# Optimization experiments

Hardware: AMD Instinct MI355X
Metric: run time of the kernel (lower is better)

The kernel has to match this reference:

```python
import jax, jax.numpy as jnp
import numpy as np

N_NODES = 50000
N_EDGES = 800000
IN_CH = 64
HID = 64
N_LAYERS = 3
K = 16           # num_clusters
OUT_CH = 64
MAX_DEG = 512
M_SUB = 256
F_CAT = HID * N_LAYERS  # 192, jk concat width
EPS = 1e-5


def graph_norm(x, w, b, ms):
    # PyG GraphNorm over all nodes (single graph): shift by ms*mean, scale by std
    mu = jnp.mean(x, axis=0)
    sh = x - ms * mu
    var = jnp.mean(sh * sh, axis=0)
    return w * sh / jnp.sqrt(var + EPS) + b


def _lin(k, fi, fo):
    k1, k2 = jax.random.split(k)
    lim = 1.0 / np.sqrt(fi)
    W = jax.random.uniform(k1, (fi, fo), minval=-lim, maxval=lim, dtype=jnp.float32)
    b = jax.random.uniform(k2, (fo,), minval=-lim, maxval=lim, dtype=jnp.float32)
    return W, b


def setup_inputs() -> dict:
    key = jax.random.key(0)
    ks = jax.random.split(key, 20)
    x = jax.random.randint(ks[0], (N_NODES,), 0, MAX_DEG + 1)
    edge_index = jax.random.randint(ks[1], (2, N_EDGES), 0, N_NODES)
    edge_weight = jax.random.uniform(ks[2], (N_EDGES,), dtype=jnp.float32)
    pos = jax.random.randint(ks[3], (M_SUB,), 0, N_NODES)
    subgraph_assignment = jax.random.uniform(ks[4], (M_SUB, N_NODES), dtype=jnp.float32)
    emb_table = jax.random.normal(ks[5], (MAX_DEG + 1, IN_CH), dtype=jnp.float32)
    conv_Ws, conv_bs = [], []
    for l in range(N_LAYERS):
        W, b = _lin(jax.random.fold_in(ks[6], l), IN_CH if l == 0 else HID, HID)
        conv_Ws.append(W); conv_bs.append(b)
    conv_W = jnp.stack(conv_Ws); conv_b = jnp.stack(conv_bs)
    gn_w = jnp.ones((N_LAYERS - 1, HID)) + 0.05 * jax.random.normal(ks[7], (N_LAYERS - 1, HID))
    gn_b = 0.05 * jax.random.normal(ks[8], (N_LAYERS - 1, HID))
    gn_ms = jnp.ones((N_LAYERS - 1, HID)) + 0.05 * jax.random.normal(ks[9], (N_LAYERS - 1, HID))
    gnl_w = jnp.ones((F_CAT,)) + 0.05 * jax.random.normal(ks[10], (F_CAT,))
    gnl_b = 0.05 * jax.random.normal(ks[11], (F_CAT,))
    gnl_ms = jnp.ones((F_CAT,)) + 0.05 * jax.random.normal(ks[12], (F_CAT,))
    emb_gn_w = jnp.ones((IN_CH,)) + 0.05 * jax.random.normal(ks[13], (IN_CH,))
    emb_gn_b = 0.05 * jax.random.normal(ks[14], (IN_CH,))
    emb_gn_ms = jnp.ones((IN_CH,)) + 0.05 * jax.random.normal(ks[15], (IN_CH,))
    s_W, s_b = _lin(ks[16], F_CAT, K)
    pin = (F_CAT + 1) * K
    p_W1, p_b1 = _lin(jax.random.fold_in(ks[17], 0), pin, 2 * HID)
    p_W2, p_b2 = _lin(jax.random.fold_in(ks[17], 1), 2 * HID, 2 * HID)
    p_W3, p_b3 = _lin(jax.random.fold_in(ks[17], 2), 2 * HID, 2 * HID)
    p_W4, p_b4 = _lin(jax.random.fold_in(ks[17], 3), 2 * HID, OUT_CH)
    return dict(x=x, edge_index=edge_index, edge_weight=edge_weight, pos=pos,
                subgraph_assignment=subgraph_assignment, emb_table=emb_table,
                emb_gn_w=emb_gn_w, emb_gn_b=emb_gn_b, emb_gn_ms=emb_gn_ms,
                conv_W=conv_W, conv_b=conv_b, gn_w=gn_w, gn_b=gn_b, gn_ms=gn_ms,
                gnl_w=gnl_w, gnl_b=gnl_b, gnl_ms=gnl_ms, s_W=s_W, s_b=s_b,
                p_W1=p_W1, p_b1=p_b1, p_W2=p_W2, p_b2=p_b2,
                p_W3=p_W3, p_b3=p_b3, p_W4=p_W4, p_b4=p_b4)


def reference(x, edge_index, edge_weight, pos, subgraph_assignment,
              emb_table, emb_gn_w, emb_gn_b, emb_gn_ms,
              conv_W, conv_b, gn_w, gn_b, gn_ms,
              gnl_w, gnl_b, gnl_ms, s_W, s_b,
              p_W1, p_b1, p_W2, p_b2, p_W3, p_b3, p_W4, p_b4):
    n = x.shape[0]
    row, col = edge_index[0], edge_index[1]
    # buildAdj, aggr='mean': row-normalized weights with zero-degree bump
    deg_raw = jax.ops.segment_sum(edge_weight, row, num_segments=n)
    deg = jnp.where(deg_raw < 0.5, deg_raw + 1.0, deg_raw)
    norm_w = edge_weight / deg[row]
    # input embedding + GraphNorm
    h = graph_norm(emb_table[x], emb_gn_w, emb_gn_b, emb_gn_ms)
    xs = []
    for l in range(N_LAYERS):
        # GLASSConv: relu(Linear(x)) then normalized-adj SpMM (dropout off: eval)
        h = jax.nn.relu(h @ conv_W[l] + conv_b[l])
        h = jax.ops.segment_sum(norm_w[:, None] * h[col], row, num_segments=n)
        xs.append(h)
        if l < N_LAYERS - 1:
            h = jax.nn.relu(graph_norm(h, gn_w[l], gn_b[l], gn_ms[l]))
    hcat = graph_norm(jnp.concatenate(xs, axis=-1), gnl_w, gnl_b, gnl_ms)  # [N, F_CAT]
    s = hcat @ s_W + s_b                       # [N, K] cluster logits
    s_sm = jax.nn.softmax(s, axis=-1)
    # dense_mincut_pool (losses via edge list == dense adj formulation)
    out = s_sm.T @ hcat                        # [K, F_CAT]
    mincut_num = jnp.sum(edge_weight * jnp.sum(s_sm[row] * s_sm[col], axis=-1))
    mincut_den = jnp.sum(deg_raw * jnp.sum(s_sm * s_sm, axis=-1))
    mc_loss = -(mincut_num / mincut_den)
    ss = s_sm.T @ s_sm                         # [K, K]
    o_loss = jnp.linalg.norm(ss / jnp.linalg.norm(ss) - jnp.eye(K) / jnp.sqrt(K))
    # subgraph -> cluster soft assignment: L1-normalize softmax(s)^T rows
    t = s_sm.T
    t = t / jnp.maximum(jnp.sum(jnp.abs(t), axis=1, keepdims=True), 1e-12)
    sub2clu = t @ subgraph_assignment.T        # [K, M]
    def pool_one(r):
        # concat cluster score column, sort clusters by score descending, flatten
        xcat = jnp.concatenate([out, r[:, None]], axis=-1)  # [K, F_CAT+1]
        return xcat[jnp.argsort(-r)].reshape(-1)
    emb = jax.vmap(pool_one)(sub2clu.T)        # [M, K*(F_CAT+1)]
    h1 = jax.nn.relu(emb @ p_W1 + p_b1)
    h2 = jax.nn.relu(h1 @ p_W2 + p_b2)
    h3 = jax.nn.relu(h2 @ p_W3 + p_b3)
    pred = h3 @ p_W4 + p_b4                    # [M, OUT_CH]
    return pred, mc_loss, o_loss
```

## Files before the change

kernel.cpp:

```cpp
#include <hip/hip_runtime.h>
#include <hip/hip_bf16.h>

using bf16 = __hip_bfloat16;

constexpr int NN  = 50000;
constexpr int NE  = 800000;
constexpr int MS  = 256;
constexpr int FC  = 192;
constexpr int KC  = 16;
constexpr int PIN = 3088;
constexpr double EPSC = 1e-5;

static __device__ __forceinline__ double ldv(const bf16* p, size_t i){ return (double)__bfloat162float(p[i]); }
static __device__ __forceinline__ double ldv(const float* p, size_t i){ return (double)p[i]; }

__global__ void k_probe(const unsigned int* __restrict__ w, int* __restrict__ flag){
  __shared__ int red[256];
  int t=threadIdx.x, mx=0;
  for (int k=t;k<512;k+=256){
    unsigned int v=w[k];
    int e=(int)((v>>7)&0xFF);
    mx = e>mx? e:mx;
  }
  red[t]=mx; __syncthreads();
  for (int s=128;s;s>>=1){ if(t<s) red[t]=max(red[t],red[t+s]); __syncthreads(); }
  if (t==0) *flag = (red[0] <= 140) ? 1 : 0;
}

struct Seg { const void* src; double* dst; float* dstf; int cnt; int off; };
struct CvtArgs { Seg s[24]; int n; int total; };
__global__ void k_convert(CvtArgs a, const int* __restrict__ flag){
  int f=*flag;
  int stride=gridDim.x*blockDim.x;
  for (int idx=blockIdx.x*blockDim.x+threadIdx.x; idx<a.total; idx+=stride){
    int lo=0;
    while (idx >= a.s[lo].off + a.s[lo].cnt) lo++;
    int j = idx - a.s[lo].off;
    double v = f ? (double)__bfloat162float(((const bf16*)a.s[lo].src)[j])
                 : (double)((const float*)a.s[lo].src)[j];
    a.s[lo].dst[j]=v;
    if (a.s[lo].dstf) a.s[lo].dstf[j]=(float)v;
  }
}

__global__ void k_reduce_d(const double* __restrict__ part, int nb, int C, double* __restrict__ out){
  __shared__ double sh[256];
  int c=blockIdx.x;
  int t=threadIdx.x;
  double s=0.0;
  for (int b=t;b<nb;b+=256) s+=part[(size_t)b*C+c];
  sh[t]=s; __syncthreads();
  for (int w=128;w;w>>=1){ if(t<w) sh[t]+=sh[t+w]; __syncthreads(); }
  if (t==0) out[c]=sh[0];
}

__global__ void k_cnt(const int* __restrict__ ei, int* __restrict__ cnt){
  int stride=gridDim.x*blockDim.x;
  for (int e=blockIdx.x*blockDim.x+threadIdx.x; e<NE; e+=stride)
    atomicAdd(&cnt[ei[e]],1);
}

__global__ void k_scan_a(const int* __restrict__ cnt, int* __restrict__ rowptr,
                         int* __restrict__ bsum){
  __shared__ int s[256];
  int t=threadIdx.x; int i=blockIdx.x*256+t;
  int v=(i<NN)?cnt[i]:0;
  s[t]=v; __syncthreads();
  for (int off=1;off<256;off<<=1){
    int x=(t>=off)?s[t-off]:0; __syncthreads();
    s[t]+=x; __syncthreads();
  }
  if (i<NN) rowptr[i]=s[t]-v;
  if (t==255) bsum[blockIdx.x]=s[255];
}
__global__ void k_scan_b(int* __restrict__ bsum, int nb){
  __shared__ int s[256];
  int t=threadIdx.x;
  int v=(t<nb)?bsum[t]:0;
  s[t]=v; __syncthreads();
  for (int off=1;off<256;off<<=1){
    int x=(t>=off)?s[t-off]:0; __syncthreads();
    s[t]+=x; __syncthreads();
  }
  if (t<nb) bsum[t]=s[t]-v;
}
__global__ void k_scan_c(int* __restrict__ rowptr, const int* __restrict__ bsum,
                         int* __restrict__ cursor){
  int i=blockIdx.x*256+threadIdx.x;
  if (i<NN){ int v=rowptr[i]+bsum[blockIdx.x]; rowptr[i]=v; cursor[i]=v; }
  if (i==0) rowptr[NN]=NE;
}

template<typename T>
__device__ __forceinline__ void scat_body(const int* __restrict__ ei, const T* __restrict__ ew,
                                          int* __restrict__ cursor, int* __restrict__ ccol,
                                          double* __restrict__ cw, int* __restrict__ ceid){
  int stride=gridDim.x*blockDim.x;
  for (int e=blockIdx.x*blockDim.x+threadIdx.x; e<NE; e+=stride){
    int r=ei[e], c=ei[NE+e];
    int p=atomicAdd(&cursor[r],1);
    ccol[p]=c; cw[p]=ldv(ew,e); ceid[p]=e;
  }
}
__global__ void k_scatter(const int* ei, const void* ew, const int* flag,
                          int* cursor, int* ccol, double* cw, int* ceid){
  if (*flag) scat_body(ei,(const bf16*)ew,cursor,ccol,cw,ceid);
  else       scat_body(ei,(const float*)ew,cursor,ccol,cw,ceid);
}

__global__ void k_rowfix(const int* __restrict__ rowptr, int* __restrict__ ccol,
                         double* __restrict__ cw, int* __restrict__ ceid,
                         double* __restrict__ deg){
  int r=blockIdx.x*blockDim.x+threadIdx.x;
  if (r>=NN) return;
  int r0=rowptr[r], r1=rowptr[r+1];
  for (int k=r0;k<r1;k++){
    int best=ceid[k], bi=k;
    for (int e=k+1;e<r1;e++){ int id=ceid[e]; if (id<best){best=id;bi=e;} }
    if (bi!=k){
      int te=ceid[k]; ceid[k]=ceid[bi]; ceid[bi]=te;
      int tc=ccol[k]; ccol[k]=ccol[bi]; ccol[bi]=tc;
      double tw=cw[k]; cw[k]=cw[bi]; cw[bi]=tw;
    }
  }
  double d=0.0;
  for (int k=r0;k<r1;k++) d+=cw[k];
  deg[r]=d;
  double dn=(d<0.5)?d+1.0:d;
  for (int k=r0;k<r1;k++) cw[k]=cw[k]/dn;
}

__global__ void k_emb(const int* __restrict__ x, const double* __restrict__ tab,
                      double* __restrict__ h, double* __restrict__ part){
  __shared__ double r1[256], r2[256];
  int t=threadIdx.x; int stride=gridDim.x*blockDim.x;
  double s1=0.0,s2=0.0;
  for (int idx=blockIdx.x*blockDim.x+t; idx<NN*64; idx+=stride){
    int i=idx>>6, c=idx&63;
    double v=tab[x[i]*64+c];
    h[idx]=v; s1+=v; s2+=v*v;
  }
  r1[t]=s1; r2[t]=s2; __syncthreads();
  if (t<64){
    double a=r1[t]+r1[t+64]+r1[t+128]+r1[t+192];
    double b=r2[t]+r2[t+64]+r2[t+128]+r2[t+192];
    part[(size_t)blockIdx.x*128+t]=a;
    part[(size_t)blockIdx.x*128+64+t]=b;
  }
}

__global__ void k_gnfin(const double* __restrict__ S,
                        const double* __restrict__ w, const double* __restrict__ b,
                        const double* __restrict__ ms, int C,
                        double* __restrict__ A, double* __restrict__ B){
  int c=threadIdx.x; if (c>=C) return;
  const double inv_n=1.0/(double)NN;
  double m1=S[c]*inv_n, ex2=S[c+C]*inv_n;
  double cc=ms[c]*m1;
  double var=ex2-2.0*cc*m1+cc*cc;
  double a=w[c]/sqrt(var+EPSC);
  A[c]=a; B[c]=b[c]-a*cc;
}

__global__ void k_gnfin_jk(const double* __restrict__ S3,
                           const double* __restrict__ w, const double* __restrict__ b,
                           const double* __restrict__ ms,
                           double* __restrict__ A, double* __restrict__ B){
  int c=threadIdx.x; if (c>=192) return;
  int l=c>>6, cc=c&63;
  const double inv_n=1.0/(double)NN;
  double m1=S3[l*128+cc]*inv_n, ex2=S3[l*128+64+cc]*inv_n;
  double m=ms[c]*m1;
  double var=ex2-2.0*m*m1+m*m;
  double a=w[c]/sqrt(var+EPSC);
  A[c]=a; B[c]=b[c]-a*m;
}

__global__ void __launch_bounds__(256) k_lin64gn(
        const double* __restrict__ X, int ldx, int cx, int inRelu,
        const double* __restrict__ A, const double* __restrict__ Bb,
        const double* __restrict__ W, const double* __restrict__ bias,
        double* __restrict__ out){
  __shared__ double Wl[4096];
  __shared__ double Al[64], Bl[64];
  int t=threadIdx.x;
  for (int i=t;i<4096;i+=256) Wl[i]=W[i];
  if (t<64){ Al[t]=A[t]; Bl[t]=Bb[t]; }
  __syncthreads();
  int lane=t&63;
  int wid=blockIdx.x*4+(t>>6);
  int nw=gridDim.x*4;
  double bj=bias[lane];
  for (int i=wid;i<NN;i+=nw){
    const double* hr=X+(size_t)i*ldx+cx;
    double acc=bj;
    #pragma unroll 8
    for (int k=0;k<64;k++){
      double v=Al[k]*hr[k]+Bl[k];
      if (inRelu) v=fmax(v,0.0);
      acc+=v*Wl[k*64+lane];
    }
    out[(size_t)i*64+lane]=fmax(acc,0.0);
  }
}

__global__ void k_spmm(const int* __restrict__ rowptr, const int* __restrict__ ccol,
                       const double* __restrict__ cw, const double* __restrict__ tin,
                       double* __restrict__ hcat, int c0, double* __restrict__ pcs){
  __shared__ double sh1[4][64], sh2[4][64];
  int lane=threadIdx.x&63, w=threadIdx.x>>6;
  int wid=blockIdx.x*4+w;
  int nw=gridDim.x*4;
  double s1=0.0, s2=0.0;
  for (int i=wid;i<NN;i+=nw){
    int r0=rowptr[i], r1=rowptr[i+1];
    double acc=0.0;
    for (int e=r0;e<r1;e++){
      int c=ccol[e]; double wv=cw[e];
      acc+=wv*tin[(size_t)c*64+lane];
    }
    hcat[(size_t)i*192+c0+lane]=acc;
    s1+=acc; s2+=acc*acc;
  }
  sh1[w][lane]=s1; sh2[w][lane]=s2;
  __syncthreads();
  if (threadIdx.x<64){
    double a=sh1[0][lane]+sh1[1][lane]+sh1[2][lane]+sh1[3][lane];
    double b=sh2[0][lane]+sh2[1][lane]+sh2[2][lane]+sh2[3][lane];
    pcs[(size_t)blockIdx.x*128+lane]=a;
    pcs[(size_t)blockIdx.x*128+64+lane]=b;
  }
}

__global__ void k_smax(const double* __restrict__ hcat,
                       const double* __restrict__ A, const double* __restrict__ B,
                       const double* __restrict__ sW, const double* __restrict__ sb,
                       const double* __restrict__ deg,
                       double* __restrict__ ssm, float* __restrict__ ssmf,
                       double* __restrict__ part){
  __shared__ double Wl[FC*KC];
  __shared__ double Al[FC], Bl[FC];
  __shared__ double redd[256];
  int t=threadIdx.x;
  for (int idx=t; idx<FC*KC; idx+=256) Wl[idx]=sW[idx];
  if (t<FC){ Al[t]=A[t]; Bl[t]=B[t]; }
  __syncthreads();
  int j=t&15, g=t>>4;
  double bj=sb[j];
  double rs=0.0, dn=0.0;
  for (int i=blockIdx.x*16+g; i<NN; i+=gridDim.x*16){
    const double* hr=hcat+(size_t)i*FC;
    double s=bj;
    #pragma unroll 8
    for (int k=0;k<FC;k++){
      double v=Al[k]*hr[k]+Bl[k];
      s+=v*Wl[k*16+j];
    }
    double m=s;
    #pragma unroll
    for (int o=8;o;o>>=1) m=fmax(m,__shfl_xor(m,o,16));
    double ev=exp(s-m), sm=ev;
    #pragma unroll
    for (int o=8;o;o>>=1) sm+=__shfl_xor(sm,o,16);
    double p=ev/sm;
    ssm[(size_t)i*16+j]=p;
    ssmf[(size_t)i*16+j]=(float)p;
    rs+=p;
    double q=p*p;
    #pragma unroll
    for (int o=8;o;o>>=1) q+=__shfl_xor(q,o,16);
    if (j==0) dn+=deg[i]*q;
  }
  redd[t]=rs; __syncthreads();
  if (t<16){ double s=0.0; for(int u=t;u<256;u+=16) s+=redd[u]; part[(size_t)blockIdx.x*17+t]=s; }
  __syncthreads(); redd[t]=dn; __syncthreads();
  if (t==0){ double s=0.0; for(int u=0;u<256;u++) s+=redd[u]; part[(size_t)blockIdx.x*17+16]=s; }
}

__global__ void k_outacc(const double* __restrict__ hcat,
                         const double* __restrict__ A, const double* __restrict__ B,
                         const double* __restrict__ ssm, double* __restrict__ part){
  int t=threadIdx.x;
  double At=A[t], Bt=B[t];
  double acc[16];
  #pragma unroll
  for (int j=0;j<16;j++) acc[j]=0.0;
  for (int i=blockIdx.x;i<NN;i+=gridDim.x){
    double hv=At*hcat[(size_t)i*FC+t]+Bt;
    const double* sr=ssm+(size_t)i*16;
    #pragma unroll
    for (int j=0;j<16;j++) acc[j]+=hv*sr[j];
  }
  #pragma unroll
  for (int j=0;j<16;j++) part[(size_t)blockIdx.x*3072 + j*FC + t]=acc[j];
}

__global__ void k_ssacc(const float* __restrict__ ssmf, double* __restrict__ part){
  int t=threadIdx.x; int j1=t>>4, j2=t&15;
  double acc=0.0;
  for (int i=blockIdx.x;i<NN;i+=gridDim.x)
    acc+=(double)(ssmf[(size_t)i*16+j1]*ssmf[(size_t)i*16+j2]);
  part[(size_t)blockIdx.x*256+t]=acc;
}

template<typename T>
__device__ __forceinline__ void mincut_body(const int* __restrict__ ei, const T* __restrict__ ew,
                                            const float* __restrict__ ssmf, double* __restrict__ part){
  int stride=gridDim.x*blockDim.x;
  double acc=0.0;
  for (int e=blockIdx.x*blockDim.x+threadIdx.x; e<NE; e+=stride){
    int r=ei[e], c=ei[NE+e];
    const float4* a=reinterpret_cast<const float4*>(ssmf+(size_t)r*16);
    const float4* b=reinterpret_cast<const float4*>(ssmf+(size_t)c*16);
    float d=0.f;
    #pragma unroll
    for (int q=0;q<4;q++){ float4 xx=a[q],yy=b[q]; d+=xx.x*yy.x+xx.y*yy.y+xx.z*yy.z+xx.w*yy.w; }
    acc+=ldv(ew,e)*(double)d;
  }
  #pragma unroll
  for (int o=32;o;o>>=1) acc+=__shfl_down(acc,o);
  __shared__ double r4[4];
  if ((threadIdx.x&63)==0) r4[threadIdx.x>>6]=acc;
  __syncthreads();
  if (threadIdx.x==0) part[blockIdx.x]=r4[0]+r4[1]+r4[2]+r4[3];
}
__global__ void k_mincut(const int* ei, const void* ew, const int* flag,
                         const float* ssmf, double* part){
  if (*flag) mincut_body(ei,(const bf16*)ew,ssmf,part);
  else       mincut_body(ei,(const float*)ew,ssmf,part);
}

__global__ void k_final(const double* __restrict__ ssa, const double* __restrict__ num,
                        const double* __restrict__ rowden, double* __restrict__ tn,
                        void* __restrict__ outv, const int* __restrict__ flag){
  __shared__ double red[256];
  int t=threadIdx.x;
  if (t<16) tn[t]=1.0/fmax(rowden[t],1e-12);
  double v=ssa[t];
  red[t]=v*v; __syncthreads();
  for (int s=128;s;s>>=1){ if(t<s) red[t]+=red[t+s]; __syncthreads(); }
  double nrm=sqrt(red[0]); __syncthreads();
  double d=v/nrm - (((t>>4)==(t&15))?0.25:0.0);
  red[t]=d*d; __syncthreads();
  for (int s=128;s;s>>=1){ if(t<s) red[t]+=red[t+s]; __syncthreads(); }
  if (t==0){
    double mc=-num[0]/rowden[16];
    double ol=sqrt(red[0]);
    if (*flag){
      bf16* o=(bf16*)outv;
      o[16384]=__float2bfloat16((float)mc); o[16385]=__float2bfloat16((float)ol);
    } else {
      float* o=(float*)outv;
      o[16384]=(float)mc; o[16385]=(float)ol;
    }
  }
}

template<typename T>
__device__ __forceinline__ void s2c_body(const double* __restrict__ ssm, const T* __restrict__ sga,
                                         double* __restrict__ ps2c){
  int t=threadIdx.x;
  int mg = blockIdx.x & 15, chunk = blockIdx.x >> 4;
  int m0 = mg*16;
  int i0 = chunk*391, i1 = min(i0+391, NN);
  int il = t>>4, j = t&15;
  double acc[16];
  #pragma unroll
  for (int mm=0;mm<16;mm++) acc[mm]=0.0;
  for (int i=i0+il; i<i1; i+=16){
    double sv = ssm[(size_t)i*16 + j];
    #pragma unroll
    for (int mm=0;mm<16;mm++)
      acc[mm] += ldv(sga,(size_t)(m0+mm)*NN + i) * sv;
  }
  #pragma unroll
  for (int mm=0;mm<16;mm++){
    double v=acc[mm];
    v += __shfl_xor(v,16,64);
    v += __shfl_xor(v,32,64);
    acc[mm]=v;
  }
  __shared__ double red[4][16][16];
  int w=t>>6;
  if ((t&48)==0){
    #pragma unroll
    for (int mm=0;mm<16;mm++) red[w][mm][j]=acc[mm];
  }
  __syncthreads();
  int mm=t>>4, j2=t&15;
  double s = red[0][mm][j2]+red[1][mm][j2]+red[2][mm][j2]+red[3][mm][j2];
  ps2c[(size_t)blockIdx.x*256 + mm*16 + j2] = s;
}
__global__ void k_sub2clu(const double* ssm, const void* sga, const int* flag,
                          double* ps2c){
  if (*flag) s2c_body(ssm,(const bf16*)sga,ps2c);
  else       s2c_body(ssm,(const float*)sga,ps2c);
}
__global__ void k_s2cfin(const double* __restrict__ ps2c, const double* __restrict__ tn,
                         double* __restrict__ s2c){
  int t=threadIdx.x;
  int mg=blockIdx.x, mm=t>>4, j=t&15;
  double s=0.0;
  for (int ch=0; ch<128; ch++)
    s += ps2c[((size_t)(ch*16+mg))*256 + mm*16 + j];
  s2c[(mg*16+mm)*16 + j] = tn[j]*s;
}

__global__ void k_findswap(const double* __restrict__ s2c, int* __restrict__ swp){
  __shared__ double gmin[256];
  __shared__ int ginf[256];
  int m=threadIdx.x;
  double r[16];
  #pragma unroll
  for (int j=0;j<16;j++) r[j]=s2c[m*16+j];
  int rank[16], ord[16];
  #pragma unroll
  for (int t2=0;t2<16;t2++){
    double rv=r[t2]; int rk=0;
    #pragma unroll
    for (int j=0;j<16;j++) rk += (r[j]>rv) || (r[j]==rv && j<t2);
    rank[t2]=rk;
  }
  #pragma unroll
  for (int j=0;j<16;j++) ord[rank[j]]=j;
  double best=1e300; int ba=0, bb=0;
  #pragma unroll
  for (int p=0;p<15;p++){
    double g=fabs(r[ord[p]]-r[ord[p+1]]);
    if (g<best){ best=g; ba=ord[p]; bb=ord[p+1]; }
  }
  gmin[m]=best; ginf[m]=(m<<8)|(ba<<4)|bb;
  __syncthreads();
  for (int s=128;s;s>>=1){
    if (m<s){
      if (gmin[m+s]<gmin[m] || (gmin[m+s]==gmin[m] && ginf[m+s]<ginf[m])){
        gmin[m]=gmin[m+s]; ginf[m]=ginf[m+s];
      }
    }
    __syncthreads();
  }
  if (m==0){
    if (gmin[0] < 1e-6){
      swp[0]=ginf[0]>>8; swp[1]=(ginf[0]>>4)&15; swp[2]=ginf[0]&15;
    } else { swp[0]=-1; swp[1]=0; swp[2]=0; }
  }
}

__global__ void k_poolsort(const double* __restrict__ s2c, const double* __restrict__ oacc,
                           const int* __restrict__ swp, float* __restrict__ emb){
  __shared__ double r[16]; __shared__ int rank[16];
  int m=blockIdx.x, t=threadIdx.x;
  if (t<16) r[t]=s2c[m*16+t];
  __syncthreads();
  if (t<16){
    double rv=r[t]; int rk=0;
    for (int j=0;j<16;j++) rk += (r[j]>rv) || (r[j]==rv && j<t);
    rank[t]=rk;
  }
  __syncthreads();
  if (t==0 && m==swp[0]){
    int a=swp[1], b=swp[2];
    int ra=rank[a]; rank[a]=rank[b]; rank[b]=ra;
  }
  __syncthreads();
  for (int j=0;j<16;j++){
    int p=rank[j];
    if (t<192)       emb[(size_t)m*PIN + p*193 + t]   = (float)oacc[j*FC+t];
    else if (t==192) emb[(size_t)m*PIN + p*193 + 192] = (float)r[j];
  }
}

__global__ void k_mlp1(const float* __restrict__ emb, const float* __restrict__ W1,
                       float* __restrict__ part){
  int t=threadIdx.x;
  int mg = blockIdx.x & 15, kc = blockIdx.x >> 4;
  int o = t & 127, half = t>>7;
  int m0 = mg*16 + half*8;
  int k0 = kc*193, k1 = k0+193;
  float acc[8];
  #pragma unroll
  for (int mm=0;mm<8;mm++) acc[mm]=0.f;
  for (int k=k0;k<k1;k++){
    float w = W1[(size_t)k*128+o];
    #pragma unroll
    for (int mm=0;mm<8;mm++)
      acc[mm] += emb[(size_t)(m0+mm)*PIN + k]*w;
  }
  #pragma unroll
  for (int mm=0;mm<8;mm++)
    part[((size_t)kc*256 + (m0+mm))*128 + o] = acc[mm];
}
__global__ void k_mlp1red(const float* __restrict__ part, const float* __restrict__ b1,
                          float* __restrict__ h1){
  int idx = blockIdx.x*256 + threadIdx.x;
  int m = idx>>7, o = idx&127;
  float s = b1[o];
  for (int kc=0;kc<16;kc++) s += part[((size_t)kc*256+m)*128+o];
  h1[(size_t)m*128+o]=s;
}

__global__ void k_mlptail(const float* __restrict__ h1,
                          const float* __restrict__ W2, const float* __restrict__ b2,
                          const float* __restrict__ W3, const float* __restrict__ b3,
                          const float* __restrict__ W4, const float* __restrict__ b4,
                          void* __restrict__ outv, const int* __restrict__ flag){
  __shared__ float a[128], bsh[128];
  int m=blockIdx.x, t=threadIdx.x;
  a[t]=h1[(size_t)m*128+t];
  __syncthreads();
  float acc=b2[t];
  #pragma unroll 4
  for (int k=0;k<128;k++) acc += fmaxf(a[k],0.f)*W2[k*128+t];
  bsh[t]=acc; __syncthreads();
  acc=b3[t];
  #pragma unroll 4
  for (int k=0;k<128;k++) acc += fmaxf(bsh[k],0.f)*W3[k*128+t];
  __syncthreads();
  a[t]=acc; __syncthreads();
  if (t<64){
    float o=b4[t];
    #pragma unroll 4
    for (int k=0;k<128;k++) o += fmaxf(a[k],0.f)*W4[k*64+t];
    if (*flag) ((bf16*)outv)[(size_t)m*64+t]=__float2bfloat16(o);
    else       ((float*)outv)[(size_t)m*64+t]=o;
  }
}

extern "C" void kernel_launch(void* const* d_in, const int* in_sizes, int n_in,
                              void* d_out, int out_size, void* d_ws, size_t ws_size,
                              hipStream_t stream){
  const int*  x    = (const int*)d_in[0];
  const int*  ei   = (const int*)d_in[1];
  const void* ew   = d_in[2];
  const void* sga  = d_in[4];
  const void* tab  = d_in[5];

  char* base=(char*)d_ws;
  size_t off=0;
  auto alloc=[&](size_t bytes)->void*{ size_t o=(off+15)&~(size_t)15; off=o+bytes; return (void*)(base+o); };

  int*    cnt    = (int*)   alloc(NN*4);
  int*    flag   = (int*)   alloc(16);
  int*    swp    = (int*)   alloc(16);
  int*    rowptr = (int*)   alloc((NN+1)*4);
  int*    cursor = (int*)   alloc(NN*4);
  int*    bsum   = (int*)   alloc(256*4);
  int*    ccol   = (int*)   alloc((size_t)NE*4);
  int*    ceid   = (int*)   alloc((size_t)NE*4);
  double* cwv    = (double*)alloc((size_t)NE*8);
  double* deg    = (double*)alloc(NN*8);
  double* h      = (double*)alloc((size_t)NN*64*8);
  double* tmp    = (double*)alloc((size_t)NN*64*8);
  double* hcat   = (double*)alloc((size_t)NN*FC*8);
  double* ssm    = (double*)alloc((size_t)NN*16*8);
  float*  ssmf   = (float*) alloc((size_t)NN*16*4);
  double* Abuf   = (double*)alloc(FC*8);
  double* Bbuf   = (double*)alloc(FC*8);
  double* Sbuf   = (double*)alloc(128*8);
  double* S3     = (double*)alloc(3*128*8);
  double* rowden = (double*)alloc(17*8);
  double* num    = (double*)alloc(8);
  double* ssa    = (double*)alloc(256*8);
  double* tn     = (double*)alloc(16*8);
  double* pemb   = (double*)alloc((size_t)1024*128*8);
  double* pcs    = (double*)alloc((size_t)2048*128*8);
  double* psmax  = (double*)alloc((size_t)1024*17*8);
  double* pout   = (double*)alloc((size_t)1024*3072*8);
  double* pss    = (double*)alloc((size_t)1024*256*8);
  double* pmc    = (double*)alloc(1024*8);
  double* oacc   = (double*)alloc((size_t)KC*FC*8);
  double* ps2c   = (double*)alloc((size_t)2048*256*8);
  double* s2c    = (double*)alloc((size_t)MS*16*8);
  float*  embf   = (float*) alloc((size_t)MS*PIN*4);
  float*  pml1   = (float*) alloc((size_t)16*256*128*4);
  float*  h1     = (float*) alloc((size_t)MS*128*4);
  double* Parea  = (double*)alloc((size_t)486224*8);
  float*  Pfarea = (float*) alloc((size_t)436672*4);
  (void)ws_size;(void)n_in;(void)in_sizes;(void)out_size;

  double* P=Parea;
  double* tabf=P;   P+=32832;
  double* egwf=P;   P+=64;  double* egbf=P;  P+=64;  double* egmsf=P; P+=64;
  double* cWf=P;    P+=12288; double* cbf=P; P+=192;
  double* gwf=P;    P+=128; double* gbf=P;   P+=128; double* gmsf=P;  P+=128;
  double* glwf=P;   P+=192; double* glbf=P;  P+=192; double* glmsf=P; P+=192;
  double* sWf=P;    P+=3072; double* sbf=P;  P+=16;
  double* pW1f=P;   P+=395264; double* pb1f=P; P+=128;
  double* pW2f=P;   P+=16384;  double* pb2f=P; P+=128;
  double* pW3f=P;   P+=16384;  double* pb3f=P; P+=128;
  double* pW4f=P;   P+=8192;   double* pb4f=P; P+=64;

  float* Pf=Pfarea;
  float* pW1s=Pf;  Pf+=395264; float* pb1s=Pf; Pf+=128;
  float* pW2s=Pf;  Pf+=16384;  float* pb2s=Pf; Pf+=128;
  float* pW3s=Pf;  Pf+=16384;  float* pb3s=Pf; Pf+=128;
  float* pW4s=Pf;  Pf+=8192;   float* pb4s=Pf; Pf+=64;

  hipMemsetAsync(cnt,0,NN*sizeof(int),stream);
  k_probe<<<1,256,0,stream>>>((const unsigned int*)tab,flag);

  CvtArgs ca; int nseg=0, tot=0;
  auto push=[&](const void* s, double* d, int c, float* df=nullptr){
    ca.s[nseg].src=s; ca.s[nseg].dst=d; ca.s[nseg].dstf=df; ca.s[nseg].cnt=c; ca.s[nseg].off=tot;
    nseg++; tot+=c;
  };
  push(d_in[5],tabf,32832);
  push(d_in[6],egwf,64);  push(d_in[7],egbf,64);   push(d_in[8],egmsf,64);
  push(d_in[9],cWf,12288); push(d_in[10],cbf,192);
  push(d_in[11],gwf,128);  push(d_in[12],gbf,128); push(d_in[13],gmsf,128);
  push(d_in[14],glwf,192); push(d_in[15],glbf,192); push(d_in[16],glmsf,192);
  push(d_in[17],sWf,3072); push(d_in[18],sbf,16);
  push(d_in[19],pW1f,395264,pW1s); push(d_in[20],pb1f,128,pb1s);
  push(d_in[21],pW2f,16384,pW2s);  push(d_in[22],pb2f,128,pb2s);
  push(d_in[23],pW3f,16384,pW3s);  push(d_in[24],pb3f,128,pb3s);
  push(d_in[25],pW4f,8192,pW4s);   push(d_in[26],pb4f,64,pb4s);
  ca.n=nseg; ca.total=tot;
  k_convert<<<256,256,0,stream>>>(ca,flag);

  k_cnt<<<512,256,0,stream>>>(ei,cnt);
  int nb=(NN+255)/256;
  k_scan_a<<<nb,256,0,stream>>>(cnt,rowptr,bsum);
  k_scan_b<<<1,256,0,stream>>>(bsum,nb);
  k_scan_c<<<nb,256,0,stream>>>(rowptr,bsum,cursor);
  k_scatter<<<512,256,0,stream>>>(ei,ew,flag,cursor,ccol,cwv,ceid);
  k_rowfix<<<nb,256,0,stream>>>(rowptr,ccol,cwv,ceid,deg);

  k_emb<<<1024,256,0,stream>>>(x,tabf,h,pemb);
  k_reduce_d<<<128,256,0,stream>>>(pemb,1024,128,Sbuf);
  k_gnfin<<<1,64,0,stream>>>(Sbuf,egwf,egbf,egmsf,64,Abuf,Bbuf);

  for (int l=0;l<3;l++){
    if (l==0) k_lin64gn<<<2048,256,0,stream>>>(h,64,0,0,Abuf,Bbuf,cWf,cbf,tmp);
    else      k_lin64gn<<<2048,256,0,stream>>>(hcat,192,(l-1)*64,1,Abuf,Bbuf,
                                               cWf+(size_t)l*4096,cbf+l*64,tmp);
    k_spmm<<<2048,256,0,stream>>>(rowptr,ccol,cwv,tmp,hcat,l*64,pcs);
    k_reduce_d<<<128,256,0,stream>>>(pcs,2048,128,S3+l*128);
    if (l<2)
      k_gnfin<<<1,64,0,stream>>>(S3+l*128,gwf+l*64,gbf+l*64,gmsf+l*64,64,Abuf,Bbuf);
  }

  k_gnfin_jk<<<1,192,0,stream>>>(S3,glwf,glbf,glmsf,Abuf,Bbuf);

  k_smax<<<1024,256,0,stream>>>(hcat,Abuf,Bbuf,sWf,sbf,deg,ssm,ssmf,psmax);
  k_reduce_d<<<17,256,0,stream>>>(psmax,1024,17,rowden);
  k_outacc<<<1024,192,0,stream>>>(hcat,Abuf,Bbuf,ssm,pout);
  k_reduce_d<<<3072,256,0,stream>>>(pout,1024,3072,oacc);
  k_ssacc<<<1024,256,0,stream>>>(ssmf,pss);
  k_reduce_d<<<256,256,0,stream>>>(pss,1024,256,ssa);
  k_mincut<<<1024,256,0,stream>>>(ei,ew,flag,ssmf,pmc);
  k_reduce_d<<<1,256,0,stream>>>(pmc,1024,1,num);
  k_final<<<1,256,0,stream>>>(ssa,num,rowden,tn,d_out,flag);

  k_sub2clu<<<2048,256,0,stream>>>(ssm,sga,flag,ps2c);
  k_s2cfin<<<16,256,0,stream>>>(ps2c,tn,s2c);
  k_findswap<<<1,256,0,stream>>>(s2c,swp);
  k_poolsort<<<256,256,0,stream>>>(s2c,oacc,swp,embf);
  k_mlp1<<<256,256,0,stream>>>(embf,pW1s,pml1);
  k_mlp1red<<<128,256,0,stream>>>(pml1,pb1s,h1);
  k_mlptail<<<256,128,0,stream>>>(h1,pW2s,pb2s,pW3s,pb3s,pW4s,pb4s,d_out,flag);
}
```

Baseline: 1.214 ms.

## Parallelize CSR row sort with wave-per-row rank sort; unroll SpMM edge loop

Replaces the thread-per-row selection sort in k_rowfix with one wavefront per row. Each lane computes its edge's rank by comparing edge ids in shared memory, scatters to its sorted position, and the row is normalized in parallel. A serial fallback remains for rows with more than 64 edges. Separately, the SpMM inner loop is unrolled by four with independent accumulators to expose more memory-level parallelism, which changes the floating-point summation order slightly.

Measured after the change: 1.067 ms. 12.1% less time.

```diff
diff --git a/kernel.cpp b/kernel.cpp
--- a/kernel.cpp
+++ b/kernel.cpp
@@ -111,23 +111,53 @@
 __global__ void k_rowfix(const int* __restrict__ rowptr, int* __restrict__ ccol,
                          double* __restrict__ cw, int* __restrict__ ceid,
                          double* __restrict__ deg){
-  int r=blockIdx.x*blockDim.x+threadIdx.x;
-  if (r>=NN) return;
+  __shared__ int    ids[4][64];
+  __shared__ double wls[4][64];
+  __shared__ double dns[4];
+  int w=threadIdx.x>>6, lane=threadIdx.x&63;
+  int r=blockIdx.x*4+w;
   int r0=rowptr[r], r1=rowptr[r+1];
-  for (int k=r0;k<r1;k++){
-    int best=ceid[k], bi=k;
-    for (int e=k+1;e<r1;e++){ int id=ceid[e]; if (id<best){best=id;bi=e;} }
-    if (bi!=k){
-      int te=ceid[k]; ceid[k]=ceid[bi]; ceid[bi]=te;
-      int tc=ccol[k]; ccol[k]=ccol[bi]; ccol[bi]=tc;
-      double tw=cw[k]; cw[k]=cw[bi]; cw[bi]=tw;
+  int d=r1-r0;
+  bool small=(d<=64);
+  int id=0,c=0; double wt=0.0;
+  if (small && lane<d){
+    id=ceid[r0+lane]; c=ccol[r0+lane]; wt=cw[r0+lane];
+    ids[w][lane]=id;
+  }
+  __syncthreads();
+  int rank=0;
+  if (small && lane<d){
+    for (int j=0;j<d;j++) rank += (ids[w][j] < id);
+    ceid[r0+rank]=id; ccol[r0+rank]=c;
+    wls[w][rank]=wt;
+  }
+  __syncthreads();
+  if (small){
+    if (lane==0){
+      double ds=0.0;
+      for (int k=0;k<d;k++) ds+=wls[w][k];
+      deg[r]=ds;
+      dns[w]=(ds<0.5)?ds+1.0:ds;
     }
-  }
-  double d=0.0;
-  for (int k=r0;k<r1;k++) d+=cw[k];
-  deg[r]=d;
-  double dn=(d<0.5)?d+1.0:d;
-  for (int k=r0;k<r1;k++) cw[k]=cw[k]/dn;
+  } else if (lane==0){
+    for (int k=r0;k<r1;k++){
+      int best=ceid[k], bi=k;
+      for (int e=k+1;e<r1;e++){ int idd=ceid[e]; if (idd<best){best=idd;bi=e;} }
+      if (bi!=k){
+        int te=ceid[k]; ceid[k]=ceid[bi]; ceid[bi]=te;
+        int tc=ccol[k]; ccol[k]=ccol[bi]; ccol[bi]=tc;
+        double tw=cw[k]; cw[k]=cw[bi]; cw[bi]=tw;
+      }
+    }
+    double ds=0.0;
+    for (int k=r0;k<r1;k++) ds+=cw[k];
+    deg[r]=ds;
+    double dn=(ds<0.5)?ds+1.0:ds;
+    for (int k=r0;k<r1;k++) cw[k]=cw[k]/dn;
+  }
+  __syncthreads();
+  if (small && lane<d)
+    cw[r0+rank]=wt/dns[w];
 }
 
 __global__ void k_emb(const int* __restrict__ x, const double* __restrict__ tab,
@@ -214,11 +244,19 @@
   double s1=0.0, s2=0.0;
   for (int i=wid;i<NN;i+=nw){
     int r0=rowptr[i], r1=rowptr[i+1];
-    double acc=0.0;
-    for (int e=r0;e<r1;e++){
-      int c=ccol[e]; double wv=cw[e];
-      acc+=wv*tin[(size_t)c*64+lane];
+    double a0=0.0,a1=0.0,a2=0.0,a3=0.0;
+    int e=r0;
+    for (; e+3<r1; e+=4){
+      int c_0=ccol[e], c_1=ccol[e+1], c_2=ccol[e+2], c_3=ccol[e+3];
+      double w0=cw[e], w1=cw[e+1], w2=cw[e+2], w3=cw[e+3];
+      a0+=w0*tin[(size_t)c_0*64+lane];
+      a1+=w1*tin[(size_t)c_1*64+lane];
+      a2+=w2*tin[(size_t)c_2*64+lane];
+      a3+=w3*tin[(size_t)c_3*64+lane];
     }
+    for (; e<r1; e++)
+      a0+=cw[e]*tin[(size_t)ccol[e]*64+lane];
+    double acc=((a0+a1)+(a2+a3));
     hcat[(size_t)i*192+c0+lane]=acc;
     s1+=acc; s2+=acc*acc;
   }
@@ -623,7 +661,7 @@
   k_scan_b<<<1,256,0,stream>>>(bsum,nb);
   k_scan_c<<<nb,256,0,stream>>>(rowptr,bsum,cursor);
   k_scatter<<<512,256,0,stream>>>(ei,ew,flag,cursor,ccol,cwv,ceid);
-  k_rowfix<<<nb,256,0,stream>>>(rowptr,ccol,cwv,ceid,deg);
+  k_rowfix<<<12500,256,0,stream>>>(rowptr,ccol,cwv,ceid,deg);
 
   k_emb<<<1024,256,0,stream>>>(x,tabf,h,pemb);
   k_reduce_d<<<128,256,0,stream>>>(pemb,1024,128,Sbuf);
```
